# Kernel optimization log

Hardware: AMD Instinct MI355X
Metric: run time of the kernel (lower is better)

The kernel has to match this reference:

```python
import jax, jax.numpy as jnp
import numpy as np

ALPHA = 0.2  # LeakyReLU negative slope
MASK_VAL = -9e15


def setup_inputs() -> dict:
    key = jax.random.key(0)
    k1, k2, k3, k4 = jax.random.split(key, 4)
    N, F_IN, F_OUT = 8192, 512, 64
    x = jax.random.normal(k1, (N, F_IN), dtype=jnp.float32)
    adj = jax.random.randint(k2, (N, N), 0, 2, dtype=jnp.int32)
    W = jax.random.normal(k3, (F_IN, F_OUT), dtype=jnp.float32) * (1.414 / np.sqrt(F_IN))
    a = jax.random.normal(k4, (2 * F_OUT, 1), dtype=jnp.float32) * 0.1
    return {"x": x, "adj": adj, "W": W, "a": a}


def reference(x, adj, W, a):
    # h = x @ W : [N, F_OUT]
    h = x @ W
    F_OUT = h.shape[1]
    # additive attention decomposed: score_ij = leaky_relu(a1.h_i + a2.h_j)
    # (mathematically identical to cat([h_i, h_j]) @ a, without the N^2*2F tensor)
    a1 = a[:F_OUT, 0]
    a2 = a[F_OUT:, 0]
    f1 = h @ a1  # [N]
    f2 = h @ a2  # [N]
    e = jax.nn.leaky_relu(f1[:, None] + f2[None, :], negative_slope=ALPHA)  # [N, N]
    e = jnp.where(adj > 0, e, MASK_VAL)
    attention = jax.nn.softmax(e, axis=1)  # dropout p=0.0 / eval mode -> identity
    h_prime = attention @ h  # [N, F_OUT]
    return jax.nn.elu(h_prime)  # concat=True path
```

## Files before the change

### kernel.cpp

```cpp
#include <hip/hip_runtime.h>
#include <stdint.h>

#define NN 8192
#define FIN 512
#define FOUT 64
#define ALPHA 0.2f
#define TJ 512
#define NT (NN / TJ)

typedef float f32x4 __attribute__((ext_vector_type(4)));
typedef int   i32x4 __attribute__((ext_vector_type(4)));
typedef short bf16x8 __attribute__((ext_vector_type(8)));

__device__ __forceinline__ unsigned short f2bf(float f) {
  union { float f; unsigned u; } v; v.f = f;
  unsigned r = (v.u + 0x7fffu + ((v.u >> 16) & 1u)) >> 16;
  return (unsigned short)r;
}

__device__ __forceinline__ unsigned packbits(i32x4 a, i32x4 b) {
  unsigned r = 0;
#pragma unroll
  for (int e = 0; e < 4; ++e) r |= (a[e] > 0 ? 1u : 0u) << e;
#pragma unroll
  for (int e = 0; e < 4; ++e) r |= (b[e] > 0 ? 1u : 0u) << (4 + e);
  return r;
}

__global__ __launch_bounds__(256) void compact_kernel(
    const int* __restrict__ adj, unsigned char* __restrict__ bits) {
  const int lane = threadIdx.x & 63;
  const int wid = blockIdx.x * 4 + (threadIdx.x >> 6);
  const int* p0 = adj + (size_t)wid * 2048 + lane * 8;

  i32x4 va0 = *(const i32x4*)(p0);
  i32x4 vb0 = *(const i32x4*)(p0 + 4);
  i32x4 va1 = *(const i32x4*)(p0 + 512);
  i32x4 vb1 = *(const i32x4*)(p0 + 516);
  i32x4 va2 = *(const i32x4*)(p0 + 1024);
  i32x4 vb2 = *(const i32x4*)(p0 + 1028);
  i32x4 va3 = *(const i32x4*)(p0 + 1536);
  i32x4 vb3 = *(const i32x4*)(p0 + 1540);

  unsigned char* ob = bits + (size_t)wid * 256 + lane;
  ob[0]   = (unsigned char)packbits(va0, vb0);
  ob[64]  = (unsigned char)packbits(va1, vb1);
  ob[128] = (unsigned char)packbits(va2, vb2);
  ob[192] = (unsigned char)packbits(va3, vb3);
}

__global__ __launch_bounds__(256) void prep_kernel(
    const float* __restrict__ x, const float* __restrict__ W,
    const float* __restrict__ a, unsigned short* __restrict__ bpack,
    float* __restrict__ f1, float* __restrict__ f2) {
  const int lane = threadIdx.x & 63;
  const int g = blockIdx.x * 4 + (threadIdx.x >> 6);
  const int i0 = g * 8;

  float acc[8];
#pragma unroll
  for (int r = 0; r < 8; ++r) acc[r] = 0.0f;

  for (int k = 0; k < FIN; k += 4) {
    float w0 = W[(k + 0) * FOUT + lane];
    float w1 = W[(k + 1) * FOUT + lane];
    float w2 = W[(k + 2) * FOUT + lane];
    float w3 = W[(k + 3) * FOUT + lane];
#pragma unroll
    for (int r = 0; r < 8; ++r) {
      f32x4 xv = *(const f32x4*)(x + (size_t)(i0 + r) * FIN + k);
      acc[r] = fmaf(xv[0], w0, acc[r]);
      acc[r] = fmaf(xv[1], w1, acc[r]);
      acc[r] = fmaf(xv[2], w2, acc[r]);
      acc[r] = fmaf(xv[3], w3, acc[r]);
    }
  }

  const float a1c = a[lane];
  const float a2c = a[FOUT + lane];
#pragma unroll
  for (int r = 0; r < 8; ++r) {
    float p1 = acc[r] * a1c;
    float p2 = acc[r] * a2c;
#pragma unroll
    for (int off = 32; off >= 1; off >>= 1) {
      p1 += __shfl_xor(p1, off, 64);
      p2 += __shfl_xor(p2, off, 64);
    }
    if (lane == 0) { f1[i0 + r] = p1; f2[i0 + r] = p2; }
  }

  unsigned short hs[8];
#pragma unroll
  for (int r = 0; r < 8; ++r) hs[r] = f2bf(acc[r]);
  const int jb = i0 >> 5;
  const int kg = (i0 >> 3) & 3;
  const int cb = lane >> 4;
  const int rr = lane & 15;
  *(uint4*)(bpack + ((size_t)jb * 2048 + cb * 512 + kg * 128 + rr * 8)) = *(uint4*)hs;
}

__global__ __launch_bounds__(1024, 4) void attn_kernel(
    const unsigned char* __restrict__ bits, const unsigned short* __restrict__ bpack,
    const float* __restrict__ f1, const float* __restrict__ f2,
    float* __restrict__ out) {
  __shared__ __align__(16) char lds[16 * 16 * 64 * 4];
  __shared__ float lds_den[16];

  char* pwb0 = lds;
  char* pwb1 = lds + 16384;
  float (*lds_num)[16][64] = (float (*)[16][64])lds;

  const int tid = threadIdx.x;
  const int lane = tid & 63;
  const int wv = tid >> 6;
  const int rg = blockIdx.x;
  const int r15 = lane & 15;
  const int kgrp = lane >> 4;

  const int row_w = rg * 16 + wv;
  const float f1w = f1[row_w];
  const unsigned char* bitsrow = bits + (size_t)row_w * (NN / 8);

  int ard = r15 * 1024 + wv * 64 + kgrp * 16;
  ard ^= (r15 & 7) << 4;
  int awr = wv * 1024 + lane * 16;
  awr ^= (wv & 7) << 4;

  f32x4 acc0 = {0.f, 0.f, 0.f, 0.f};
  f32x4 acc1 = acc0, acc2 = acc0, acc3 = acc0;
  float den = 0.0f;

  unsigned bcur = bitsrow[lane];
  f32x4 fA = *(const f32x4*)(f2 + lane * 8);
  f32x4 fB = *(const f32x4*)(f2 + lane * 8 + 4);

  for (int t = 0; t < NT; ++t) {
    const unsigned short* bp = bpack + ((size_t)(t * 16 + wv) * 2048 + lane * 8);
    bf16x8 b0 = *(const bf16x8*)(bp);
    bf16x8 b1 = *(const bf16x8*)(bp + 512);
    bf16x8 b2 = *(const bf16x8*)(bp + 1024);
    bf16x8 b3 = *(const bf16x8*)(bp + 1536);

    const int tn = (t + 1) & (NT - 1);
    unsigned bnxt = bitsrow[tn * 64 + lane];
    f32x4 nfA = *(const f32x4*)(f2 + tn * TJ + lane * 8);
    f32x4 nfB = *(const f32x4*)(f2 + tn * TJ + lane * 8 + 4);

    unsigned short ws8[8];
    float dsum = 0.0f;
#pragma unroll
    for (int e = 0; e < 4; ++e) {
      float s = f1w + fA[e];
      float l = fmaxf(s, ALPHA * s);
      float ev = __expf(l);
      float w_ = ((bcur >> e) & 1u) ? ev : 0.0f;
      dsum += w_;
      ws8[e] = f2bf(w_);
    }
#pragma unroll
    for (int e = 0; e < 4; ++e) {
      float s = f1w + fB[e];
      float l = fmaxf(s, ALPHA * s);
      float ev = __expf(l);
      float w_ = ((bcur >> (4 + e)) & 1u) ? ev : 0.0f;
      dsum += w_;
      ws8[4 + e] = f2bf(w_);
    }
    den += dsum;

    char* pwb = (t & 1) ? pwb1 : pwb0;
    *(uint4*)(pwb + awr) = *(uint4*)ws8;

    __syncthreads();

    bf16x8 afrag = *(bf16x8*)(pwb + ard);
    acc0 = __builtin_amdgcn_mfma_f32_16x16x32_bf16(afrag, b0, acc0, 0, 0, 0);
    acc1 = __builtin_amdgcn_mfma_f32_16x16x32_bf16(afrag, b1, acc1, 0, 0, 0);
    acc2 = __builtin_amdgcn_mfma_f32_16x16x32_bf16(afrag, b2, acc2, 0, 0, 0);
    acc3 = __builtin_amdgcn_mfma_f32_16x16x32_bf16(afrag, b3, acc3, 0, 0, 0);

    bcur = bnxt; fA = nfA; fB = nfB;
  }

#pragma unroll
  for (int off = 1; off <= 32; off <<= 1) den += __shfl_xor(den, off, 64);

  __syncthreads();

#pragma unroll
  for (int r = 0; r < 4; ++r) {
    lds_num[wv][kgrp * 4 + r][0 * 16 + r15] = acc0[r];
    lds_num[wv][kgrp * 4 + r][1 * 16 + r15] = acc1[r];
    lds_num[wv][kgrp * 4 + r][2 * 16 + r15] = acc2[r];
    lds_num[wv][kgrp * 4 + r][3 * 16 + r15] = acc3[r];
  }
  if (lane == 0) lds_den[wv] = den;
  __syncthreads();

  {
    const int orow = tid >> 6;
    const int ocol = tid & 63;
    float s = 0.0f;
#pragma unroll
    for (int v = 0; v < 16; ++v) s += lds_num[v][orow][ocol];
    float vv = s / lds_den[orow];
    out[(size_t)(rg * 16 + orow) * FOUT + ocol] = (vv > 0.0f) ? vv : (__expf(vv) - 1.0f);
  }
}

extern "C" void kernel_launch(void* const* d_in, const int* in_sizes, int n_in,
                              void* d_out, int out_size, void* d_ws, size_t ws_size,
                              hipStream_t stream) {
  const float* x = (const float*)d_in[0];
  const int* adj = (const int*)d_in[1];
  const float* W = (const float*)d_in[2];
  const float* a = (const float*)d_in[3];
  float* out = (float*)d_out;

  char* ws = (char*)d_ws;
  unsigned short* bpack = (unsigned short*)ws;
  float* f1 = (float*)(ws + (size_t)FOUT * NN * 2);
  float* f2 = f1 + NN;
  unsigned char* bits = (unsigned char*)(ws + (2u << 20));

  hipLaunchKernelGGL(compact_kernel, dim3(8192), dim3(256), 0, stream, adj, bits);
  hipLaunchKernelGGL(prep_kernel, dim3(256), dim3(256), 0, stream, x, W, a, bpack, f1, f2);
  hipLaunchKernelGGL(attn_kernel, dim3(512), dim3(1024), 0, stream, bits, bpack, f1, f2, out);
}
```

Measured before the change: 127.0 us.

## Fuse prep kernels and factor exp into precomputed per-node terms with bigger row blocks

Merges the adjacency bit-compaction and the projection kernel into a single launch. It also precomputes exp(f2), exp(alpha*f2), exp(-f1) and exp(-0.8*f1), so the attention weight becomes a compare plus a multiply instead of a per-element exp. The attention kernel now handles 32 rows per block with 512 threads and 8 MFMA accumulators. The f2-exp tiles are staged through LDS with double-buffered B fragments, and raw s_barrier is used in place of __syncthreads. The factored exponentials can overflow or underflow for large-magnitude scores, since there is no max subtraction.

```diff
diff --git a/kernel.cpp b/kernel.cpp
--- a/kernel.cpp
+++ b/kernel.cpp
@@ -1,23 +1,20 @@
 #include <hip/hip_runtime.h>
+#include <hip/hip_bf16.h>
 #include <stdint.h>
 
 #define NN 8192
 #define FIN 512
 #define FOUT 64
 #define ALPHA 0.2f
-#define TJ 512
+#define TJ 256
 #define NT (NN / TJ)
+#define RB 32
+#define NBLK (NN / RB)
 
 typedef float f32x4 __attribute__((ext_vector_type(4)));
 typedef int   i32x4 __attribute__((ext_vector_type(4)));
 typedef short bf16x8 __attribute__((ext_vector_type(8)));
 
-__device__ __forceinline__ unsigned short f2bf(float f) {
-  union { float f; unsigned u; } v; v.f = f;
-  unsigned r = (v.u + 0x7fffu + ((v.u >> 16) & 1u)) >> 16;
-  return (unsigned short)r;
-}
-
 __device__ __forceinline__ unsigned packbits(i32x4 a, i32x4 b) {
   unsigned r = 0;
 #pragma unroll
@@ -27,34 +24,37 @@
   return r;
 }
 
-__global__ __launch_bounds__(256) void compact_kernel(
-    const int* __restrict__ adj, unsigned char* __restrict__ bits) {
+__global__ __launch_bounds__(256) void stream_kernel(
+    const int* __restrict__ adj, const float* __restrict__ x,
+    const float* __restrict__ W, const float* __restrict__ a,
+    unsigned char* __restrict__ bits, unsigned short* __restrict__ bpack,
+    float* __restrict__ er, float* __restrict__ rr,
+    float* __restrict__ e2p, float* __restrict__ e2n) {
   const int lane = threadIdx.x & 63;
-  const int wid = blockIdx.x * 4 + (threadIdx.x >> 6);
-  const int* p0 = adj + (size_t)wid * 2048 + lane * 8;
-
-  i32x4 va0 = *(const i32x4*)(p0);
-  i32x4 vb0 = *(const i32x4*)(p0 + 4);
-  i32x4 va1 = *(const i32x4*)(p0 + 512);
-  i32x4 vb1 = *(const i32x4*)(p0 + 516);
-  i32x4 va2 = *(const i32x4*)(p0 + 1024);
-  i32x4 vb2 = *(const i32x4*)(p0 + 1028);
-  i32x4 va3 = *(const i32x4*)(p0 + 1536);
-  i32x4 vb3 = *(const i32x4*)(p0 + 1540);
-
-  unsigned char* ob = bits + (size_t)wid * 256 + lane;
-  ob[0]   = (unsigned char)packbits(va0, vb0);
-  ob[64]  = (unsigned char)packbits(va1, vb1);
-  ob[128] = (unsigned char)packbits(va2, vb2);
-  ob[192] = (unsigned char)packbits(va3, vb3);
-}
-
-__global__ __launch_bounds__(256) void prep_kernel(
-    const float* __restrict__ x, const float* __restrict__ W,
-    const float* __restrict__ a, unsigned short* __restrict__ bpack,
-    float* __restrict__ f1, float* __restrict__ f2) {
-  const int lane = threadIdx.x & 63;
-  const int g = blockIdx.x * 4 + (threadIdx.x >> 6);
+  const int bid = blockIdx.x;
+
+  if (bid < 8192) {
+    const int wid = bid * 4 + (threadIdx.x >> 6);
+    const int* p0 = adj + (size_t)wid * 2048 + lane * 8;
+
+    i32x4 va0 = *(const i32x4*)(p0);
+    i32x4 vb0 = *(const i32x4*)(p0 + 4);
+    i32x4 va1 = *(const i32x4*)(p0 + 512);
+    i32x4 vb1 = *(const i32x4*)(p0 + 516);
+    i32x4 va2 = *(const i32x4*)(p0 + 1024);
+    i32x4 vb2 = *(const i32x4*)(p0 + 1028);
+    i32x4 va3 = *(const i32x4*)(p0 + 1536);
+    i32x4 vb3 = *(const i32x4*)(p0 + 1540);
+
+    unsigned char* ob = bits + (size_t)wid * 256 + lane;
+    ob[0]   = (unsigned char)packbits(va0, vb0);
+    ob[64]  = (unsigned char)packbits(va1, vb1);
+    ob[128] = (unsigned char)packbits(va2, vb2);
+    ob[192] = (unsigned char)packbits(va3, vb3);
+    return;
+  }
+
+  const int g = (bid - 8192) * 4 + (threadIdx.x >> 6);
   const int i0 = g * 8;
 
   float acc[8];
@@ -87,29 +87,33 @@
       p1 += __shfl_xor(p1, off, 64);
       p2 += __shfl_xor(p2, off, 64);
     }
-    if (lane == 0) { f1[i0 + r] = p1; f2[i0 + r] = p2; }
+    if (lane == 0) {
+      er[i0 + r] = __expf(-p1);
+      rr[i0 + r] = __expf(-0.8f * p1);
+      e2p[i0 + r] = __expf(p2);
+      e2n[i0 + r] = __expf(ALPHA * p2);
+    }
   }
 
   unsigned short hs[8];
 #pragma unroll
-  for (int r = 0; r < 8; ++r) hs[r] = f2bf(acc[r]);
+  for (int r = 0; r < 8; ++r) {
+    __hip_bfloat16 hb = __float2bfloat16(acc[r]);
+    hs[r] = *reinterpret_cast<unsigned short*>(&hb);
+  }
   const int jb = i0 >> 5;
   const int kg = (i0 >> 3) & 3;
   const int cb = lane >> 4;
-  const int rr = lane & 15;
-  *(uint4*)(bpack + ((size_t)jb * 2048 + cb * 512 + kg * 128 + rr * 8)) = *(uint4*)hs;
-}
-
-__global__ __launch_bounds__(1024, 4) void attn_kernel(
+  const int rrr = lane & 15;
+  *(uint4*)(bpack + ((size_t)jb * 2048 + cb * 512 + kg * 128 + rrr * 8)) = *(uint4*)hs;
+}
+
+__global__ __launch_bounds__(512, 2) void attn_kernel(
     const unsigned char* __restrict__ bits, const unsigned short* __restrict__ bpack,
-    const float* __restrict__ f1, const float* __restrict__ f2,
+    const float* __restrict__ er, const float* __restrict__ rr,
+    const float* __restrict__ e2p, const float* __restrict__ e2n,
     float* __restrict__ out) {
-  __shared__ __align__(16) char lds[16 * 16 * 64 * 4];
-  __shared__ float lds_den[16];
-
-  char* pwb0 = lds;
-  char* pwb1 = lds + 16384;
-  float (*lds_num)[16][64] = (float (*)[16][64])lds;
+  __shared__ __align__(16) char lds[65536 + 128];
 
   const int tid = threadIdx.x;
   const int lane = tid & 63;
@@ -117,95 +121,150 @@
   const int rg = blockIdx.x;
   const int r15 = lane & 15;
   const int kgrp = lane >> 4;
-
-  const int row_w = rg * 16 + wv;
-  const float f1w = f1[row_w];
-  const unsigned char* bitsrow = bits + (size_t)row_w * (NN / 8);
-
-  int ard = r15 * 1024 + wv * 64 + kgrp * 16;
-  ard ^= (r15 & 7) << 4;
-  int awr = wv * 1024 + lane * 16;
-  awr ^= (wv & 7) << 4;
-
-  f32x4 acc0 = {0.f, 0.f, 0.f, 0.f};
-  f32x4 acc1 = acc0, acc2 = acc0, acc3 = acc0;
+  const int jl = r15;
+  const int qr = kgrp;
+
+  const int wrow = wv * 4 + qr;
+  const int growr = rg * RB + wrow;
+  const float er_v = er[growr];
+  const float rr_v = rr[growr];
+  const unsigned char* brow = bits + (size_t)growr * (NN / 8);
+
+  f32x4 acc00 = {0.f,0.f,0.f,0.f}, acc01 = acc00, acc02 = acc00, acc03 = acc00;
+  f32x4 acc10 = acc00, acc11 = acc00, acc12 = acc00, acc13 = acc00;
   float den = 0.0f;
 
-  unsigned bcur = bitsrow[lane];
-  f32x4 fA = *(const f32x4*)(f2 + lane * 8);
-  f32x4 fB = *(const f32x4*)(f2 + lane * 8 + 4);
-
-  for (int t = 0; t < NT; ++t) {
-    const unsigned short* bp = bpack + ((size_t)(t * 16 + wv) * 2048 + lane * 8);
-    bf16x8 b0 = *(const bf16x8*)(bp);
-    bf16x8 b1 = *(const bf16x8*)(bp + 512);
-    bf16x8 b2 = *(const bf16x8*)(bp + 1024);
-    bf16x8 b3 = *(const bf16x8*)(bp + 1536);
-
-    const int tn = (t + 1) & (NT - 1);
-    unsigned bnxt = bitsrow[tn * 64 + lane];
-    f32x4 nfA = *(const f32x4*)(f2 + tn * TJ + lane * 8);
-    f32x4 nfB = *(const f32x4*)(f2 + tn * TJ + lane * 8 + 4);
-
-    unsigned short ws8[8];
-    float dsum = 0.0f;
-#pragma unroll
-    for (int e = 0; e < 4; ++e) {
-      float s = f1w + fA[e];
-      float l = fmaxf(s, ALPHA * s);
-      float ev = __expf(l);
-      float w_ = ((bcur >> e) & 1u) ? ev : 0.0f;
-      dsum += w_;
-      ws8[e] = f2bf(w_);
-    }
-#pragma unroll
-    for (int e = 0; e < 4; ++e) {
-      float s = f1w + fB[e];
-      float l = fmaxf(s, ALPHA * s);
-      float ev = __expf(l);
-      float w_ = ((bcur >> (4 + e)) & 1u) ? ev : 0.0f;
-      dsum += w_;
-      ws8[4 + e] = f2bf(w_);
-    }
-    den += dsum;
-
-    char* pwb = (t & 1) ? pwb1 : pwb0;
-    *(uint4*)(pwb + awr) = *(uint4*)ws8;
-
-    __syncthreads();
-
-    bf16x8 afrag = *(bf16x8*)(pwb + ard);
-    acc0 = __builtin_amdgcn_mfma_f32_16x16x32_bf16(afrag, b0, acc0, 0, 0, 0);
-    acc1 = __builtin_amdgcn_mfma_f32_16x16x32_bf16(afrag, b1, acc1, 0, 0, 0);
-    acc2 = __builtin_amdgcn_mfma_f32_16x16x32_bf16(afrag, b2, acc2, 0, 0, 0);
-    acc3 = __builtin_amdgcn_mfma_f32_16x16x32_bf16(afrag, b3, acc3, 0, 0, 0);
-
-    bcur = bnxt; fA = nfA; fB = nfB;
-  }
-
-#pragma unroll
-  for (int off = 1; off <= 32; off <<= 1) den += __shfl_xor(den, off, 64);
-
-  __syncthreads();
-
+  bf16x8 bA[4], bB[4];
+  unsigned mb;
+
+  {
+    char* eb = lds + 32768;
+    if (tid < 256) {
+      float v = e2p[tid];
+      int b = tid * 4; b ^= ((b >> 8) & 7) << 4;
+      *(float*)(eb + b) = v;
+    } else {
+      const int q_ = tid - 256;
+      float v = e2n[q_];
+      int b = q_ * 4; b ^= ((b >> 8) & 7) << 4;
+      *(float*)(eb + 1024 + b) = v;
+    }
+    const unsigned short* bp = bpack + ((size_t)(wv) * 2048) + lane * 8;
+    bA[0] = *(const bf16x8*)(bp);        bA[1] = *(const bf16x8*)(bp + 512);
+    bA[2] = *(const bf16x8*)(bp + 1024); bA[3] = *(const bf16x8*)(bp + 1536);
+    mb = *(const unsigned short*)(brow + jl * 2);
+  }
+  asm volatile("s_waitcnt lgkmcnt(0)\n\ts_barrier" ::: "memory");
+
+#define ATTN_ITER(T_, BC, BN) do { \
+    const int t_ = (T_); \
+    const int tn_ = (t_ + 1) & (NT - 1); \
+    {  \
+      char* eb = lds + 32768 + ((t_ + 1) & 1) * 2048; \
+      const int jt = tn_ * TJ; \
+      if (tid < 256) { \
+        float v = e2p[jt + tid]; \
+        int b = tid * 4; b ^= ((b >> 8) & 7) << 4; \
+        *(float*)(eb + b) = v; \
+      } else { \
+        const int q_ = tid - 256; \
+        float v = e2n[jt + q_]; \
+        int b = q_ * 4; b ^= ((b >> 8) & 7) << 4; \
+        *(float*)(eb + 1024 + b) = v; \
+      } \
+    } \
+    {  \
+      const unsigned short* bp = bpack + ((size_t)(tn_ * 8 + wv) * 2048) + lane * 8; \
+      BN[0] = *(const bf16x8*)(bp);        BN[1] = *(const bf16x8*)(bp + 512); \
+      BN[2] = *(const bf16x8*)(bp + 1024); BN[3] = *(const bf16x8*)(bp + 1536); \
+    } \
+    const unsigned mbn_ = *(const unsigned short*)(brow + tn_ * 32 + jl * 2); \
+    {  \
+      char* eb = lds + 32768 + (t_ & 1) * 2048; \
+      f32x4 ep[4], en[4]; \
+      _Pragma("unroll") \
+      for (int h = 0; h < 4; ++h) { \
+        int b = jl * 64 + h * 16; b ^= ((b >> 8) & 7) << 4; \
+        ep[h] = *(f32x4*)(eb + b); \
+        en[h] = *(f32x4*)(eb + 1024 + b); \
+      } \
+      unsigned short w8[16]; \
+      _Pragma("unroll") \
+      for (int h = 0; h < 4; ++h) { \
+        _Pragma("unroll") \
+        for (int e = 0; e < 4; ++e) { \
+          const int k = h * 4 + e; \
+          float p = ep[h][e]; \
+          float w = (p > er_v) ? p : rr_v * en[h][e]; \
+          w = ((mb >> k) & 1u) ? w : 0.0f; \
+          den += w; \
+          __hip_bfloat16 hb = __float2bfloat16(w); \
+          w8[k] = *reinterpret_cast<unsigned short*>(&hb); \
+        } \
+      } \
+      char* pwb = lds + (t_ & 1) * 16384; \
+      const int b0 = wrow * 512 + jl * 32; \
+      *(uint4*)(pwb + (b0 ^ ((wrow & 7) << 4))) = *(uint4*)&w8[0]; \
+      *(uint4*)(pwb + ((b0 + 16) ^ ((wrow & 7) << 4))) = *(uint4*)&w8[8]; \
+    } \
+    asm volatile("s_waitcnt lgkmcnt(0)\n\ts_barrier" ::: "memory"); \
+    {  \
+      char* pwb = lds + (t_ & 1) * 16384; \
+      const int bA0 = (r15 * 512 + wv * 64 + kgrp * 16) ^ ((r15 & 7) << 4); \
+      const int bA1 = ((16 + r15) * 512 + wv * 64 + kgrp * 16) ^ ((r15 & 7) << 4); \
+      bf16x8 A0 = *(bf16x8*)(pwb + bA0); \
+      bf16x8 A1 = *(bf16x8*)(pwb + bA1); \
+      acc00 = __builtin_amdgcn_mfma_f32_16x16x32_bf16(A0, BC[0], acc00, 0, 0, 0); \
+      acc01 = __builtin_amdgcn_mfma_f32_16x16x32_bf16(A0, BC[1], acc01, 0, 0, 0); \
+      acc02 = __builtin_amdgcn_mfma_f32_16x16x32_bf16(A0, BC[2], acc02, 0, 0, 0); \
+      acc03 = __builtin_amdgcn_mfma_f32_16x16x32_bf16(A0, BC[3], acc03, 0, 0, 0); \
+      acc10 = __builtin_amdgcn_mfma_f32_16x16x32_bf16(A1, BC[0], acc10, 0, 0, 0); \
+      acc11 = __builtin_amdgcn_mfma_f32_16x16x32_bf16(A1, BC[1], acc11, 0, 0, 0); \
+      acc12 = __builtin_amdgcn_mfma_f32_16x16x32_bf16(A1, BC[2], acc12, 0, 0, 0); \
+      acc13 = __builtin_amdgcn_mfma_f32_16x16x32_bf16(A1, BC[3], acc13, 0, 0, 0); \
+    } \
+    mb = mbn_; \
+  } while (0)
+
+  for (int tt = 0; tt < NT; tt += 2) {
+    ATTN_ITER(tt, bA, bB);
+    ATTN_ITER(tt + 1, bB, bA);
+  }
+#undef ATTN_ITER
+
+#pragma unroll
+  for (int off = 1; off <= 8; off <<= 1) den += __shfl_xor(den, off, 64);
+  float* dptr = (float*)(lds + 65536);
+  if (jl == 0) dptr[wrow] = den;
+
+  asm volatile("s_waitcnt lgkmcnt(0)\n\ts_barrier" ::: "memory");
+
+  float* nump = (float*)lds;
 #pragma unroll
   for (int r = 0; r < 4; ++r) {
-    lds_num[wv][kgrp * 4 + r][0 * 16 + r15] = acc0[r];
-    lds_num[wv][kgrp * 4 + r][1 * 16 + r15] = acc1[r];
-    lds_num[wv][kgrp * 4 + r][2 * 16 + r15] = acc2[r];
-    lds_num[wv][kgrp * 4 + r][3 * 16 + r15] = acc3[r];
-  }
-  if (lane == 0) lds_den[wv] = den;
-  __syncthreads();
-
-  {
-    const int orow = tid >> 6;
-    const int ocol = tid & 63;
+    const int rl0 = kgrp * 4 + r;
+    nump[(wv * 32 + rl0) * 64 +  0 + r15] = acc00[r];
+    nump[(wv * 32 + rl0) * 64 + 16 + r15] = acc01[r];
+    nump[(wv * 32 + rl0) * 64 + 32 + r15] = acc02[r];
+    nump[(wv * 32 + rl0) * 64 + 48 + r15] = acc03[r];
+    const int rl1 = 16 + rl0;
+    nump[(wv * 32 + rl1) * 64 +  0 + r15] = acc10[r];
+    nump[(wv * 32 + rl1) * 64 + 16 + r15] = acc11[r];
+    nump[(wv * 32 + rl1) * 64 + 32 + r15] = acc12[r];
+    nump[(wv * 32 + rl1) * 64 + 48 + r15] = acc13[r];
+  }
+  asm volatile("s_waitcnt lgkmcnt(0)\n\ts_barrier" ::: "memory");
+
+#pragma unroll
+  for (int p = 0; p < 4; ++p) {
+    const int idx = tid + p * 512;
+    const int orow = idx >> 6;
+    const int ocol = idx & 63;
     float s = 0.0f;
 #pragma unroll
-    for (int v = 0; v < 16; ++v) s += lds_num[v][orow][ocol];
-    float vv = s / lds_den[orow];
-    out[(size_t)(rg * 16 + orow) * FOUT + ocol] = (vv > 0.0f) ? vv : (__expf(vv) - 1.0f);
+    for (int k = 0; k < 8; ++k) s += nump[k * 2048 + orow * 64 + ocol];
+    float v = s / dptr[orow];
+    out[(size_t)(rg * RB + orow) * FOUT + ocol] = (v > 0.0f) ? v : (__expf(v) - 1.0f);
   }
 }
 
@@ -220,11 +279,14 @@
 
   char* ws = (char*)d_ws;
   unsigned short* bpack = (unsigned short*)ws;
-  float* f1 = (float*)(ws + (size_t)FOUT * NN * 2);
-  float* f2 = f1 + NN;
-  unsigned char* bits = (unsigned char*)(ws + (2u << 20));
-
-  hipLaunchKernelGGL(compact_kernel, dim3(8192), dim3(256), 0, stream, adj, bits);
-  hipLaunchKernelGGL(prep_kernel, dim3(256), dim3(256), 0, stream, x, W, a, bpack, f1, f2);
-  hipLaunchKernelGGL(attn_kernel, dim3(512), dim3(1024), 0, stream, bits, bpack, f1, f2, out);
-}
+  float* er  = (float*)(ws + 0x100000);
+  float* rr  = (float*)(ws + 0x108000);
+  float* e2p = (float*)(ws + 0x110000);
+  float* e2n = (float*)(ws + 0x118000);
+  unsigned char* bits = (unsigned char*)(ws + 0x200000);
+
+  hipLaunchKernelGGL(stream_kernel, dim3(8192 + 256), dim3(256), 0, stream,
+                     adj, x, W, a, bits, bpack, er, rr, e2p, e2n);
+  hipLaunchKernelGGL(attn_kernel, dim3(NBLK), dim3(512), 0, stream,
+                     bits, bpack, er, rr, e2p, e2n, out);
+}
```

New measurement: 171.1 us. 34.7% more time.
